# Kernel optimization log

Measured on AMD Instinct MI355X. Metric: run time of the kernel, lower is better.

Reference implementation:

```python
import jax, jax.numpy as jnp
import numpy as np

MAX_NUM_LEVELS = 3.5
NUM_LEVELS = 4  # mip levels 0..3 (levels clamped to [0, 2.5])


def affine_grid(matrix, N, H, W):
    # F.affine_grid, align_corners=False. matrix: (N,2,3) -> grid (N,H,W,2) in xy order.
    xs = (jnp.arange(W, dtype=jnp.float32) + 0.5) * (2.0 / W) - 1.0
    ys = (jnp.arange(H, dtype=jnp.float32) + 0.5) * (2.0 / H) - 1.0
    gy, gx = jnp.meshgrid(ys, xs, indexing='ij')
    base = jnp.stack([gx, gy, jnp.ones_like(gx)], axis=-1)  # (H,W,3)
    return jnp.einsum('hwk,nik->nhwi', base, matrix)  # (N,H,W,2)


def grid_sample_border(img, grid):
    # bilinear grid_sample, padding_mode='border', align_corners=False
    N, C, H, W = img.shape
    x = (grid[..., 0] + 1.0) * (W / 2.0) - 0.5
    y = (grid[..., 1] + 1.0) * (H / 2.0) - 0.5
    x0 = jnp.floor(x); y0 = jnp.floor(y)
    tx = x - x0; ty = y - y0
    x0i = jnp.clip(x0.astype(jnp.int32), 0, W - 1)
    x1i = jnp.clip(x0.astype(jnp.int32) + 1, 0, W - 1)
    y0i = jnp.clip(y0.astype(jnp.int32), 0, H - 1)
    y1i = jnp.clip(y0.astype(jnp.int32) + 1, 0, H - 1)
    b = jnp.arange(N)[:, None, None]
    g = lambda yi, xi: img[b, :, yi, xi]  # (N,Ho,Wo,C) gather
    out = (g(y0i, x0i) * ((1 - tx) * (1 - ty))[..., None]
           + g(y0i, x1i) * (tx * (1 - ty))[..., None]
           + g(y1i, x0i) * ((1 - tx) * ty)[..., None]
           + g(y1i, x1i) * (tx * ty)[..., None])
    return jnp.transpose(out, (0, 3, 1, 2))  # (N,C,Ho,Wo)


def blur_downsample(x):
    N, C, H, W = x.shape
    k1 = jnp.array([1., 3., 3., 1.], dtype=x.dtype) / 8.0
    k = k1[:, None] * k1[None, :]
    xp = jnp.pad(x, ((0, 0), (0, 0), (1, 2), (1, 2)), mode='reflect')
    kernel = jnp.broadcast_to(k[None, None], (C, 1, 4, 4))
    return jax.lax.conv_general_dilated(xp, kernel, window_strides=(2, 2), padding='VALID',
                                        feature_group_count=C,
                                        dimension_numbers=('NCHW', 'OIHW', 'NCHW'))


def compute_levels(grid, H, W):
    # per-pixel mip LOD from local stretch of the sampling grid (in source pixel units)
    coords = (grid + 1.0) * 0.5 * jnp.array([W, H], dtype=grid.dtype)  # (N,Ho,Wo,2)
    dx = coords[:, :-1, 1:] - coords[:, :-1, :-1]
    dy = coords[:, 1:, :-1] - coords[:, :-1, :-1]
    scale = jnp.maximum(jnp.linalg.norm(dx, axis=-1), jnp.linalg.norm(dy, axis=-1))
    scale = jnp.pad(scale, ((0, 0), (0, 1), (0, 1)), mode='edge')  # (N,Ho,Wo)
    levels = jnp.log2(jnp.maximum(scale, 1.0))
    return jnp.clip(levels, 0.0, MAX_NUM_LEVELS - 1.0)


def mipmap_warp(img, grid):
    N, C, H, W = img.shape
    levels = compute_levels(grid, H, W)  # (N,Ho,Wo)
    pyr = [img]
    for _ in range(NUM_LEVELS - 1):
        pyr.append(blur_downsample(pyr[-1]))
    samples = jnp.stack([grid_sample_border(p, grid) for p in pyr], axis=0)  # (L,N,C,Ho,Wo)
    ls = jnp.arange(NUM_LEVELS, dtype=levels.dtype)[:, None, None, None]
    w = jnp.clip(1.0 - jnp.abs(levels[None] - ls), 0.0, 1.0)  # trilinear blend weights (L,N,Ho,Wo)
    return jnp.einsum('lnhw,lnchw->nchw', w, samples)


def setup_inputs() -> dict:
    key = jax.random.key(0)
    k1, k2, k3 = jax.random.split(key, 3)
    N, C, H, W, D = 64, 3, 256, 256, 512
    img = jax.random.normal(k1, (N, C, H, W), dtype=jnp.float32)
    features = jax.random.normal(k2, (N, D), dtype=jnp.float32)
    # learned head params (zero-init in torch; small random here so the warp is nontrivial)
    lin_w = jax.random.normal(k3, (4, D), dtype=jnp.float32) * 0.02
    lin_b = jnp.zeros((4,), dtype=jnp.float32)
    return {'img': img, 'features': features, 'lin_w': lin_w, 'lin_b': lin_b}


def reference(img, features, lin_w, lin_b):
    params = features @ lin_w.T + lin_b  # (N,4)
    rot = jnp.tanh(params[:, 0:1]) * jnp.pi
    scale = jnp.exp(params[:, 1:2])
    sx, sy = params[:, 2:3], params[:, 3:4]
    c, s = jnp.cos(rot), jnp.sin(rot)
    matrix = jnp.concatenate([scale * c, -scale * s, sx, scale * s, scale * c, sy], axis=1).reshape(-1, 2, 3)
    affine_params = jnp.concatenate([rot, scale, sx, sy], axis=1)
    N, C, H, W = img.shape
    grid = affine_grid(matrix, N, H, W)
    out = mipmap_warp(img, grid)
    return out, grid, matrix, affine_params
```

## Files before the change

### kernel.cpp

```cpp
#include <hip/hip_runtime.h>
#include <math.h>

#define N_B 64
#define C_CH 3
#define H_IMG 256
#define W_IMG 256
#define D_FEAT 512

#define OUT_OFF_GRID   12582912
#define OUT_OFF_MATRIX 20971520
#define OUT_OFF_AFFINE 20971904

typedef float v2f __attribute__((ext_vector_type(2)));

__global__ void params_kernel(const float* __restrict__ features,
                              const float* __restrict__ lin_w,
                              const float* __restrict__ lin_b,
                              float* __restrict__ out_matrix,
                              float* __restrict__ out_affine,
                              float* __restrict__ ws_params)
{
    const int n = blockIdx.x;
    const int t = threadIdx.x;
    const float* f = features + n * D_FEAT;
    float f0 = f[t];
    float f1 = f[t + 256];
    float a0 = f0 * lin_w[0 * D_FEAT + t] + f1 * lin_w[0 * D_FEAT + t + 256];
    float a1 = f0 * lin_w[1 * D_FEAT + t] + f1 * lin_w[1 * D_FEAT + t + 256];
    float a2 = f0 * lin_w[2 * D_FEAT + t] + f1 * lin_w[2 * D_FEAT + t + 256];
    float a3 = f0 * lin_w[3 * D_FEAT + t] + f1 * lin_w[3 * D_FEAT + t + 256];

    __shared__ float red[4][256];
    red[0][t] = a0; red[1][t] = a1; red[2][t] = a2; red[3][t] = a3;
    __syncthreads();
    for (int s = 128; s > 0; s >>= 1) {
        if (t < s) {
            red[0][t] += red[0][t + s];
            red[1][t] += red[1][t + s];
            red[2][t] += red[2][t + s];
            red[3][t] += red[3][t + s];
        }
        __syncthreads();
    }
    if (t == 0) {
        float p0 = red[0][0] + lin_b[0];
        float p1 = red[1][0] + lin_b[1];
        float p2 = red[2][0] + lin_b[2];
        float p3 = red[3][0] + lin_b[3];
        float rot   = tanhf(p0) * 3.14159265358979323846f;
        float scale = expf(p1);
        float c = cosf(rot), s = sinf(rot);
        float m00 = scale * c, m01 = -scale * s, m02 = p2;
        float m10 = scale * s, m11 =  scale * c, m12 = p3;
        out_matrix[n * 6 + 0] = m00;
        out_matrix[n * 6 + 1] = m01;
        out_matrix[n * 6 + 2] = m02;
        out_matrix[n * 6 + 3] = m10;
        out_matrix[n * 6 + 4] = m11;
        out_matrix[n * 6 + 5] = m12;
        out_affine[n * 4 + 0] = rot;
        out_affine[n * 4 + 1] = scale;
        out_affine[n * 4 + 2] = p2;
        out_affine[n * 4 + 3] = p3;
        float lv = log2f(fmaxf(scale, 1.0f));
        lv = fminf(fmaxf(lv, 0.0f), 2.5f);
        ws_params[n * 8 + 0] = m00;
        ws_params[n * 8 + 1] = m01;
        ws_params[n * 8 + 2] = m02;
        ws_params[n * 8 + 3] = m10;
        ws_params[n * 8 + 4] = m11;
        ws_params[n * 8 + 5] = m12;
        ws_params[n * 8 + 6] = lv;
        ws_params[n * 8 + 7] = 0.0f;
    }
}

template<int Hs, int Ws>
__global__ void down_kernel(const float* __restrict__ src, float* __restrict__ dst,
                            const float* __restrict__ ws_params, float lvl_gate)
{
    constexpr int Hd = Hs / 2, Wd = Ws / 2;
    constexpr int QUADS = Wd / 4;

    const int idx = blockIdx.x * blockDim.x + threadIdx.x;
    const int nc  = idx / (QUADS * Hd);
    const int n   = nc / C_CH;

    if (ws_params[n * 8 + 6] <= lvl_gate) return;

    const int t   = idx & (QUADS - 1);
    const int i   = (idx / QUADS) & (Hd - 1);

    const float* __restrict__ s = src + (size_t)nc * Hs * Ws;

    int r[4];
#pragma unroll
    for (int a = 0; a < 4; a++) {
        int q = 2 * i + a - 1;
        if (q < 0) q = -q;
        if (q >= Hs) q = 2 * Hs - 2 - q;
        r[a] = q;
    }
    const int c8 = 8 * t;
    const int li = (t > 0)         ? c8 - 1 : 1;
    const int ri = (t < QUADS - 1) ? c8 + 8 : Ws - 2;

    const float k0 = 0.125f, k1 = 0.375f;
    const float kr[4] = {0.125f, 0.375f, 0.375f, 0.125f};

    float acc0 = 0.f, acc1 = 0.f, acc2 = 0.f, acc3 = 0.f;
#pragma unroll
    for (int a = 0; a < 4; a++) {
        const float* row = s + (size_t)r[a] * Ws;
        float4 A = *(const float4*)(row + c8);
        float4 B = *(const float4*)(row + c8 + 4);
        float L = row[li];
        float R = row[ri];
        float h0 = k0 * L   + k1 * A.x + k1 * A.y + k0 * A.z;
        float h1 = k0 * A.y + k1 * A.z + k1 * A.w + k0 * B.x;
        float h2 = k0 * A.w + k1 * B.x + k1 * B.y + k0 * B.z;
        float h3 = k0 * B.y + k1 * B.z + k1 * B.w + k0 * R;
        acc0 += kr[a] * h0;
        acc1 += kr[a] * h1;
        acc2 += kr[a] * h2;
        acc3 += kr[a] * h3;
    }
    float4* d4 = (float4*)(dst + (size_t)nc * Hd * Wd + (size_t)i * Wd + 4 * t);
    *d4 = make_float4(acc0, acc1, acc2, acc3);
}

__device__ __forceinline__ const float* lvl_ptr(int l, const float* img,
                                                const float* p1, const float* p2,
                                                const float* p3)
{
    return (l == 0) ? img : ((l == 1) ? p1 : ((l == 2) ? p2 : p3));
}

struct TapSetup {
    const float* row0;
    const float* row1;
    float w00, w01, w10, w11;
    bool selHi0, selLo1;
    size_t planeStride;
};

__device__ __forceinline__ TapSetup make_taps(const float* __restrict__ base, int l,
                                              float X, float Y)
{
    const int Wl = W_IMG >> l;
    const int Hl = H_IMG >> l;
    float x = (X + 1.0f) * (0.5f * (float)Wl) - 0.5f;
    float y = (Y + 1.0f) * (0.5f * (float)Hl) - 0.5f;
    float x0f = floorf(x), y0f = floorf(y);
    float tx = x - x0f, ty = y - y0f;
    int x0 = (int)x0f, y0 = (int)y0f;
    int y0i = min(max(y0,     0), Hl - 1);
    int y1i = min(max(y0 + 1, 0), Hl - 1);
    int xp = min(max(x0, 0), Wl - 2);
    TapSetup ts;
    ts.row0 = base + (size_t)y0i * Wl + xp;
    ts.row1 = base + (size_t)y1i * Wl + xp;
    ts.selHi0 = (x0 >= Wl - 1);
    ts.selLo1 = (x0 < 0);
    ts.w00 = (1.0f - tx) * (1.0f - ty);
    ts.w01 = tx * (1.0f - ty);
    ts.w10 = (1.0f - tx) * ty;
    ts.w11 = tx * ty;
    ts.planeStride = (size_t)Hl * Wl;
    return ts;
}

__device__ __forceinline__ float tap_eval(const TapSetup& ts, float2 a, float2 b)
{
    float t00 = ts.selHi0 ? a.y : a.x;
    float t01 = ts.selLo1 ? a.x : a.y;
    float t10 = ts.selHi0 ? b.y : b.x;
    float t11 = ts.selLo1 ? b.x : b.y;
    return ts.w00 * t00 + ts.w01 * t01 + ts.w10 * t10 + ts.w11 * t11;
}

__global__ __launch_bounds__(256, 4)
void warp_kernel(const float* __restrict__ img,
                 const float* __restrict__ pyr1,
                 const float* __restrict__ pyr2,
                 const float* __restrict__ pyr3,
                 const float* __restrict__ ws_params,
                 float* __restrict__ out,
                 float* __restrict__ gridOut)
{
    const int n = blockIdx.y;
    const int tile = blockIdx.x;
    const int tid = threadIdx.x;
    const int w0 = (tile & 7) << 5;
    const int h0 = (tile >> 3) << 3;
    const int w = w0 + (((tid >> 6) & 1) << 4) + (tid & 15);
    const int h = h0 + ((tid >> 7) << 2) + ((tid >> 4) & 3);

    const float* P = ws_params + n * 8;
    float m00 = P[0], m01 = P[1], m02 = P[2];
    float m10 = P[3], m11 = P[4], m12 = P[5];
    float lv  = P[6];

    float gx = ((float)w + 0.5f) * (2.0f / (float)W_IMG) - 1.0f;
    float gy = ((float)h + 0.5f) * (2.0f / (float)H_IMG) - 1.0f;
    float X = m00 * gx + m01 * gy + m02;
    float Y = m10 * gx + m11 * gy + m12;

    v2f gp = {X, Y};
    __builtin_nontemporal_store(gp, (v2f*)gridOut + ((size_t)(n * H_IMG + h) * W_IMG + w));

    int   l0   = (int)lv;
    float frac = lv - (float)l0;
    const bool hasL1 = (frac > 0.0f);

    const int Hl0 = H_IMG >> l0, Wl0 = W_IMG >> l0;
    const float* base0 = lvl_ptr(l0, img, pyr1, pyr2, pyr3)
                       + (size_t)n * C_CH * Hl0 * Wl0;
    TapSetup t0 = make_taps(base0, l0, X, Y);

    float2 A0[C_CH], B0[C_CH];
#pragma unroll
    for (int c = 0; c < C_CH; c++) {
        A0[c] = *(const float2*)(t0.row0 + c * t0.planeStride);
        B0[c] = *(const float2*)(t0.row1 + c * t0.planeStride);
    }

    size_t obase = ((size_t)n * C_CH * H_IMG + h) * W_IMG + w;

    if (hasL1) {
        const int Hl1 = H_IMG >> (l0 + 1), Wl1 = W_IMG >> (l0 + 1);
        const float* base1 = lvl_ptr(l0 + 1, img, pyr1, pyr2, pyr3)
                           + (size_t)n * C_CH * Hl1 * Wl1;
        TapSetup t1 = make_taps(base1, l0 + 1, X, Y);

        float2 A1[C_CH], B1[C_CH];
#pragma unroll
        for (int c = 0; c < C_CH; c++) {
            A1[c] = *(const float2*)(t1.row0 + c * t1.planeStride);
            B1[c] = *(const float2*)(t1.row1 + c * t1.planeStride);
        }

        float wA = 1.0f - frac;
#pragma unroll
        for (int c = 0; c < C_CH; c++) {
            float v0 = tap_eval(t0, A0[c], B0[c]);
            float v1 = tap_eval(t1, A1[c], B1[c]);
            out[obase + (size_t)c * H_IMG * W_IMG] = wA * v0 + frac * v1;
        }
    } else {
#pragma unroll
        for (int c = 0; c < C_CH; c++) {
            out[obase + (size_t)c * H_IMG * W_IMG] = tap_eval(t0, A0[c], B0[c]);
        }
    }
}

extern "C" void kernel_launch(void* const* d_in, const int* in_sizes, int n_in,
                              void* d_out, int out_size, void* d_ws, size_t ws_size,
                              hipStream_t stream)
{
    const float* img      = (const float*)d_in[0];
    const float* features = (const float*)d_in[1];
    const float* lin_w    = (const float*)d_in[2];
    const float* lin_b    = (const float*)d_in[3];

    float* out        = (float*)d_out;
    float* gridOut    = out + OUT_OFF_GRID;
    float* out_matrix = out + OUT_OFF_MATRIX;
    float* out_affine = out + OUT_OFF_AFFINE;

    float* ws        = (float*)d_ws;
    float* ws_params = ws;
    float* pyr1 = ws + 1024;
    float* pyr2 = pyr1 + (size_t)N_B * C_CH * 128 * 128;
    float* pyr3 = pyr2 + (size_t)N_B * C_CH * 64 * 64;

    params_kernel<<<N_B, 256, 0, stream>>>(features, lin_w, lin_b,
                                           out_matrix, out_affine, ws_params);

    int t1 = N_B * C_CH * 128 * 32;
    down_kernel<256, 256><<<t1 / 256, 256, 0, stream>>>(img,  pyr1, ws_params, 0.0f);
    int t2 = N_B * C_CH * 64 * 16;
    down_kernel<128, 128><<<t2 / 256, 256, 0, stream>>>(pyr1, pyr2, ws_params, 1.0f);
    int t3 = N_B * C_CH * 32 * 8;
    down_kernel<64, 64><<<t3 / 256, 256, 0, stream>>>(pyr2, pyr3, ws_params, 2.0f);

    warp_kernel<<<dim3(H_IMG * W_IMG / 256, N_B), 256, 0, stream>>>(
        img, pyr1, pyr2, pyr3, ws_params, out, gridOut);
}
```

Before: 172.1 us.

## Store mip pyramid levels channel-interleaved so warp taps load all channels together

Pyramid levels 1-3 are now written in an interleaved HWC layout, so a bilinear tap in the warp kernel fetches all three channels for two adjacent texels with one 16-byte and one 8-byte load per row. This replaces six separate per-channel float2 loads. The downsample kernels are rewritten to produce one output pixel with all channels per thread, and the warp output now uses nontemporal stores. The trade-off is more redundant source reads in the downsample kernels, plus unaligned vector loads.

```diff
diff --git a/kernel.cpp b/kernel.cpp
--- a/kernel.cpp
+++ b/kernel.cpp
@@ -11,7 +11,13 @@
 #define OUT_OFF_MATRIX 20971520
 #define OUT_OFF_AFFINE 20971904
 
+#define PYR1_SZ (N_B * 128 * 128 * 3)
+#define PYR2_SZ (N_B * 64 * 64 * 3)
+#define PYR3_SZ (N_B * 32 * 32 * 3)
+
 typedef float v2f __attribute__((ext_vector_type(2)));
+typedef float f4u __attribute__((ext_vector_type(4), aligned(4)));
+typedef float f2u __attribute__((ext_vector_type(2), aligned(4)));
 
 __global__ void params_kernel(const float* __restrict__ features,
                               const float* __restrict__ lin_w,
@@ -75,65 +81,111 @@
     }
 }
 
+__global__ void down1_kernel(const float* __restrict__ img,
+                             float* __restrict__ pyr1,
+                             const float* __restrict__ ws_params)
+{
+    const int n = blockIdx.y;
+    if (ws_params[n * 8 + 6] <= 0.0f) return;
+    const int p = blockIdx.x * 256 + threadIdx.x;
+    const int i = p >> 7;
+    const int j = p & 127;
+
+    int r[4];
+#pragma unroll
+    for (int a = 0; a < 4; a++) {
+        int q = 2 * i + a - 1;
+        if (q < 0) q = -q;
+        if (q >= 256) q = 510 - q;
+        r[a] = q;
+    }
+    const int  cb  = min(max(2 * j - 1, 0), 252);
+    const bool jlo = (j == 0);
+    const bool jhi = (j == 127);
+    const bool je  = jlo || jhi;
+
+    const float* s = img + (size_t)n * 3 * 65536;
+
+    f4u T[3][4];
+#pragma unroll
+    for (int c = 0; c < 3; c++)
+#pragma unroll
+        for (int a = 0; a < 4; a++)
+            T[c][a] = *(const f4u*)(s + c * 65536 + r[a] * 256 + cb);
+
+    const float k0 = 0.125f, k1 = 0.375f;
+    const float kr[4] = {0.125f, 0.375f, 0.375f, 0.125f};
+    float o[3];
+#pragma unroll
+    for (int c = 0; c < 3; c++) {
+        float acc = 0.0f;
+#pragma unroll
+        for (int a = 0; a < 4; a++) {
+            f4u A = T[c][a];
+            float t0 = je  ? A.y : A.x;
+            float t1 = jlo ? A.x : (jhi ? A.z : A.y);
+            float t2 = jlo ? A.y : (jhi ? A.w : A.z);
+            float t3 = je  ? A.z : A.w;
+            float h = k0 * t0 + k1 * t1 + k1 * t2 + k0 * t3;
+            acc += kr[a] * h;
+        }
+        o[c] = acc;
+    }
+    float* d = pyr1 + (size_t)n * (128 * 128 * 3) + (size_t)p * 3;
+    d[0] = o[0]; d[1] = o[1]; d[2] = o[2];
+}
+
 template<int Hs, int Ws>
-__global__ void down_kernel(const float* __restrict__ src, float* __restrict__ dst,
-                            const float* __restrict__ ws_params, float lvl_gate)
-{
+__global__ void downN_kernel(const float* __restrict__ src,
+                             float* __restrict__ dst,
+                             const float* __restrict__ ws_params,
+                             float lvl_gate)
+{
+    const int n = blockIdx.y;
+    if (ws_params[n * 8 + 6] <= lvl_gate) return;
     constexpr int Hd = Hs / 2, Wd = Ws / 2;
-    constexpr int QUADS = Wd / 4;
-
-    const int idx = blockIdx.x * blockDim.x + threadIdx.x;
-    const int nc  = idx / (QUADS * Hd);
-    const int n   = nc / C_CH;
-
-    if (ws_params[n * 8 + 6] <= lvl_gate) return;
-
-    const int t   = idx & (QUADS - 1);
-    const int i   = (idx / QUADS) & (Hd - 1);
-
-    const float* __restrict__ s = src + (size_t)nc * Hs * Ws;
-
-    int r[4];
+    const int p = blockIdx.x * 256 + threadIdx.x;
+    const int i = p / Wd;
+    const int j = p % Wd;
+
+    int r[4], cc[4];
 #pragma unroll
     for (int a = 0; a < 4; a++) {
         int q = 2 * i + a - 1;
         if (q < 0) q = -q;
         if (q >= Hs) q = 2 * Hs - 2 - q;
         r[a] = q;
-    }
-    const int c8 = 8 * t;
-    const int li = (t > 0)         ? c8 - 1 : 1;
-    const int ri = (t < QUADS - 1) ? c8 + 8 : Ws - 2;
+        int u = 2 * j + a - 1;
+        if (u < 0) u = -u;
+        if (u >= Ws) u = 2 * Ws - 2 - u;
+        cc[a] = u;
+    }
+    const float* s = src + (size_t)n * 3 * Hs * Ws;
+    const int rs = 3 * Ws;
+
+    f4u T[4][4];
+#pragma unroll
+    for (int a = 0; a < 4; a++)
+#pragma unroll
+        for (int b = 0; b < 4; b++)
+            T[a][b] = *(const f4u*)(s + r[a] * rs + 3 * cc[b]);
 
     const float k0 = 0.125f, k1 = 0.375f;
     const float kr[4] = {0.125f, 0.375f, 0.375f, 0.125f};
-
-    float acc0 = 0.f, acc1 = 0.f, acc2 = 0.f, acc3 = 0.f;
-#pragma unroll
-    for (int a = 0; a < 4; a++) {
-        const float* row = s + (size_t)r[a] * Ws;
-        float4 A = *(const float4*)(row + c8);
-        float4 B = *(const float4*)(row + c8 + 4);
-        float L = row[li];
-        float R = row[ri];
-        float h0 = k0 * L   + k1 * A.x + k1 * A.y + k0 * A.z;
-        float h1 = k0 * A.y + k1 * A.z + k1 * A.w + k0 * B.x;
-        float h2 = k0 * A.w + k1 * B.x + k1 * B.y + k0 * B.z;
-        float h3 = k0 * B.y + k1 * B.z + k1 * B.w + k0 * R;
-        acc0 += kr[a] * h0;
-        acc1 += kr[a] * h1;
-        acc2 += kr[a] * h2;
-        acc3 += kr[a] * h3;
-    }
-    float4* d4 = (float4*)(dst + (size_t)nc * Hd * Wd + (size_t)i * Wd + 4 * t);
-    *d4 = make_float4(acc0, acc1, acc2, acc3);
-}
-
-__device__ __forceinline__ const float* lvl_ptr(int l, const float* img,
-                                                const float* p1, const float* p2,
-                                                const float* p3)
-{
-    return (l == 0) ? img : ((l == 1) ? p1 : ((l == 2) ? p2 : p3));
+    float o[3];
+#pragma unroll
+    for (int c = 0; c < 3; c++) {
+        float acc = 0.0f;
+#pragma unroll
+        for (int a = 0; a < 4; a++) {
+            float h = k0 * T[a][0][c] + k1 * T[a][1][c]
+                    + k1 * T[a][2][c] + k0 * T[a][3][c];
+            acc += kr[a] * h;
+        }
+        o[c] = acc;
+    }
+    float* d = dst + (size_t)n * 3 * Hd * Wd + (size_t)p * 3;
+    d[0] = o[0]; d[1] = o[1]; d[2] = o[2];
 }
 
 struct TapSetup {
@@ -179,6 +231,63 @@
     return ts.w00 * t00 + ts.w01 * t01 + ts.w10 * t10 + ts.w11 * t11;
 }
 
+struct NTap {
+    const float* r0;
+    const float* r1;
+    float w00, w01, w10, w11;
+    bool hi, lo;
+};
+
+__device__ __forceinline__ NTap make_ntap(const float* __restrict__ base, int l,
+                                          float X, float Y)
+{
+    const int Wl = W_IMG >> l;
+    const int Hl = H_IMG >> l;
+    float x = (X + 1.0f) * (0.5f * (float)Wl) - 0.5f;
+    float y = (Y + 1.0f) * (0.5f * (float)Hl) - 0.5f;
+    float x0f = floorf(x), y0f = floorf(y);
+    float tx = x - x0f, ty = y - y0f;
+    int x0 = (int)x0f, y0 = (int)y0f;
+    int y0i = min(max(y0,     0), Hl - 1);
+    int y1i = min(max(y0 + 1, 0), Hl - 1);
+    int xp  = min(max(x0, 0), Wl - 2);
+    const int rs = 3 * Wl;
+    NTap t;
+    t.r0 = base + (size_t)y0i * rs + 3 * xp;
+    t.r1 = base + (size_t)y1i * rs + 3 * xp;
+    t.hi = (x0 >= Wl - 1);
+    t.lo = (x0 < 0);
+    t.w00 = (1.0f - tx) * (1.0f - ty);
+    t.w01 = tx * (1.0f - ty);
+    t.w10 = (1.0f - tx) * ty;
+    t.w11 = tx * ty;
+    return t;
+}
+
+__device__ __forceinline__ void ntap_eval(const NTap& t, f4u a, f2u a2,
+                                          f4u b, f2u b2, float* v)
+{
+    float e0[6] = {a.x, a.y, a.z, a.w, a2.x, a2.y};
+    float e1[6] = {b.x, b.y, b.z, b.w, b2.x, b2.y};
+#pragma unroll
+    for (int c = 0; c < 3; c++) {
+        float p00 = t.hi ? e0[c + 3] : e0[c];
+        float p01 = t.lo ? e0[c]     : e0[c + 3];
+        float p10 = t.hi ? e1[c + 3] : e1[c];
+        float p11 = t.lo ? e1[c]     : e1[c + 3];
+        v[c] = t.w00 * p00 + t.w01 * p01 + t.w10 * p10 + t.w11 * p11;
+    }
+}
+
+__device__ __forceinline__ const float* npyr(int l, const float* p1,
+                                             const float* p2, const float* p3,
+                                             int n)
+{
+    if (l == 1) return p1 + (size_t)n * (128 * 128 * 3);
+    if (l == 2) return p2 + (size_t)n * (64 * 64 * 3);
+    return p3 + (size_t)n * (32 * 32 * 3);
+}
+
 __global__ __launch_bounds__(256, 4)
 void warp_kernel(const float* __restrict__ img,
                  const float* __restrict__ pyr1,
@@ -212,45 +321,61 @@
     int   l0   = (int)lv;
     float frac = lv - (float)l0;
     const bool hasL1 = (frac > 0.0f);
-
-    const int Hl0 = H_IMG >> l0, Wl0 = W_IMG >> l0;
-    const float* base0 = lvl_ptr(l0, img, pyr1, pyr2, pyr3)
-                       + (size_t)n * C_CH * Hl0 * Wl0;
-    TapSetup t0 = make_taps(base0, l0, X, Y);
-
-    float2 A0[C_CH], B0[C_CH];
-#pragma unroll
-    for (int c = 0; c < C_CH; c++) {
-        A0[c] = *(const float2*)(t0.row0 + c * t0.planeStride);
-        B0[c] = *(const float2*)(t0.row1 + c * t0.planeStride);
-    }
+    const float wA = 1.0f - frac;
 
     size_t obase = ((size_t)n * C_CH * H_IMG + h) * W_IMG + w;
 
-    if (hasL1) {
-        const int Hl1 = H_IMG >> (l0 + 1), Wl1 = W_IMG >> (l0 + 1);
-        const float* base1 = lvl_ptr(l0 + 1, img, pyr1, pyr2, pyr3)
-                           + (size_t)n * C_CH * Hl1 * Wl1;
-        TapSetup t1 = make_taps(base1, l0 + 1, X, Y);
-
-        float2 A1[C_CH], B1[C_CH];
-#pragma unroll
-        for (int c = 0; c < C_CH; c++) {
-            A1[c] = *(const float2*)(t1.row0 + c * t1.planeStride);
-            B1[c] = *(const float2*)(t1.row1 + c * t1.planeStride);
-        }
-
-        float wA = 1.0f - frac;
-#pragma unroll
-        for (int c = 0; c < C_CH; c++) {
-            float v0 = tap_eval(t0, A0[c], B0[c]);
-            float v1 = tap_eval(t1, A1[c], B1[c]);
-            out[obase + (size_t)c * H_IMG * W_IMG] = wA * v0 + frac * v1;
+    if (l0 == 0) {
+        const float* base0 = img + (size_t)n * 3 * 65536;
+        TapSetup t0 = make_taps(base0, 0, X, Y);
+        float2 A0[3], B0[3];
+#pragma unroll
+        for (int c = 0; c < 3; c++) {
+            A0[c] = *(const float2*)(t0.row0 + c * t0.planeStride);
+            B0[c] = *(const float2*)(t0.row1 + c * t0.planeStride);
+        }
+        if (hasL1) {
+            NTap t1 = make_ntap(pyr1 + (size_t)n * (128 * 128 * 3), 1, X, Y);
+            f4u a = *(const f4u*)t1.r0;  f2u a2 = *(const f2u*)(t1.r0 + 4);
+            f4u b = *(const f4u*)t1.r1;  f2u b2 = *(const f2u*)(t1.r1 + 4);
+            float v1[3];
+            ntap_eval(t1, a, a2, b, b2, v1);
+#pragma unroll
+            for (int c = 0; c < 3; c++) {
+                float v0 = tap_eval(t0, A0[c], B0[c]);
+                __builtin_nontemporal_store(wA * v0 + frac * v1[c],
+                                            out + obase + (size_t)c * 65536);
+            }
+        } else {
+#pragma unroll
+            for (int c = 0; c < 3; c++)
+                __builtin_nontemporal_store(tap_eval(t0, A0[c], B0[c]),
+                                            out + obase + (size_t)c * 65536);
         }
     } else {
-#pragma unroll
-        for (int c = 0; c < C_CH; c++) {
-            out[obase + (size_t)c * H_IMG * W_IMG] = tap_eval(t0, A0[c], B0[c]);
+        const float* base0 = npyr(l0, pyr1, pyr2, pyr3, n);
+        NTap t0 = make_ntap(base0, l0, X, Y);
+        f4u a = *(const f4u*)t0.r0;  f2u a2 = *(const f2u*)(t0.r0 + 4);
+        f4u b = *(const f4u*)t0.r1;  f2u b2 = *(const f2u*)(t0.r1 + 4);
+        if (hasL1) {
+            const float* base1 = npyr(l0 + 1, pyr1, pyr2, pyr3, n);
+            NTap t1 = make_ntap(base1, l0 + 1, X, Y);
+            f4u c1 = *(const f4u*)t1.r0;  f2u c2 = *(const f2u*)(t1.r0 + 4);
+            f4u d1 = *(const f4u*)t1.r1;  f2u d2 = *(const f2u*)(t1.r1 + 4);
+            float v0[3], v1[3];
+            ntap_eval(t0, a, a2, b, b2, v0);
+            ntap_eval(t1, c1, c2, d1, d2, v1);
+#pragma unroll
+            for (int c = 0; c < 3; c++)
+                __builtin_nontemporal_store(wA * v0[c] + frac * v1[c],
+                                            out + obase + (size_t)c * 65536);
+        } else {
+            float v0[3];
+            ntap_eval(t0, a, a2, b, b2, v0);
+#pragma unroll
+            for (int c = 0; c < 3; c++)
+                __builtin_nontemporal_store(v0[c],
+                                            out + obase + (size_t)c * 65536);
         }
     }
 }
@@ -272,18 +397,15 @@
     float* ws        = (float*)d_ws;
     float* ws_params = ws;
     float* pyr1 = ws + 1024;
-    float* pyr2 = pyr1 + (size_t)N_B * C_CH * 128 * 128;
-    float* pyr3 = pyr2 + (size_t)N_B * C_CH * 64 * 64;
+    float* pyr2 = pyr1 + PYR1_SZ;
+    float* pyr3 = pyr2 + PYR2_SZ;
 
     params_kernel<<<N_B, 256, 0, stream>>>(features, lin_w, lin_b,
                                            out_matrix, out_affine, ws_params);
 
-    int t1 = N_B * C_CH * 128 * 32;
-    down_kernel<256, 256><<<t1 / 256, 256, 0, stream>>>(img,  pyr1, ws_params, 0.0f);
-    int t2 = N_B * C_CH * 64 * 16;
-    down_kernel<128, 128><<<t2 / 256, 256, 0, stream>>>(pyr1, pyr2, ws_params, 1.0f);
-    int t3 = N_B * C_CH * 32 * 8;
-    down_kernel<64, 64><<<t3 / 256, 256, 0, stream>>>(pyr2, pyr3, ws_params, 2.0f);
+    down1_kernel<<<dim3(64, N_B), 256, 0, stream>>>(img, pyr1, ws_params);
+    downN_kernel<128, 128><<<dim3(16, N_B), 256, 0, stream>>>(pyr1, pyr2, ws_params, 1.0f);
+    downN_kernel<64, 64><<<dim3(4, N_B), 256, 0, stream>>>(pyr2, pyr3, ws_params, 2.0f);
 
     warp_kernel<<<dim3(H_IMG * W_IMG / 256, N_B), 256, 0, stream>>>(
         img, pyr1, pyr2, pyr3, ws_params, out, gridOut);
```

Measured after the change: 166.7 us. -3.1%, faster.
